# Kernel tuning notes

Measured on AMD Instinct MI355X. Metric: run time of the kernel, lower is better.

## Reference

```python
import jax, jax.numpy as jnp
import numpy as np

B, N, H = 8, 2048, 256


def setup_inputs() -> dict:
    key = jax.random.key(0)
    ks = jax.random.split(key, 8)
    s = 1.0 / np.sqrt(H)
    return {
        "node": jax.random.normal(ks[0], (B, N, H), dtype=jnp.float32),
        "graph": jax.random.uniform(ks[1], (B, N, N), dtype=jnp.float32),
        "W1": jax.random.normal(ks[2], (H, H), dtype=jnp.float32) * s,
        "b1": jnp.zeros((H,), dtype=jnp.float32),
        "W2": jax.random.normal(ks[3], (H, H), dtype=jnp.float32) * s,
        "b2": jnp.zeros((H,), dtype=jnp.float32),
        "Wout": jax.random.normal(ks[4], (H, 2 * H), dtype=jnp.float32) * (1.0 / np.sqrt(2 * H)),
        "bout": jnp.zeros((H,), dtype=jnp.float32),
    }


def reference(node, graph, W1, b1, W2, b2, Wout, bout):
    # Symmetric normalization D^{-1/2} A D^{-1/2}, batched and vectorized
    # (equivalent to the per-sample diag-mm loop in the original).
    d = jnp.sum(graph, axis=2)                # [B, N] row sums (torch sum(1) on [N,N])
    dinv = d ** -0.5                          # [B, N]
    g = graph * dinv[:, :, None] * dinv[:, None, :]  # [B, N, N]

    # node_info = relu(fc1(g @ node)); fc2(g @ node_info)
    h = jax.nn.relu(jnp.einsum("bnm,bmh->bnh", g, node) @ W1.T + b1)
    h = jax.nn.relu(jnp.einsum("bnm,bmh->bnh", g, h) @ W2.T + b2)

    agg = jnp.concatenate([node, h], axis=2)  # [B, N, 2H]
    return jax.nn.relu(agg @ Wout.T + bout)   # [B, N, H]
```

## Files before the change

kernel.cpp:

```cpp
#include <hip/hip_runtime.h>
#include <stdint.h>

typedef __attribute__((ext_vector_type(4))) float f32x4;
typedef __attribute__((ext_vector_type(8))) short bf16x8;

static __device__ __forceinline__ unsigned short f2bf(float x) {
  unsigned int u = __builtin_bit_cast(unsigned int, x);
  u = (u + 0x7fffu + ((u >> 16) & 1u)) >> 16;
  return (unsigned short)u;
}

#define GLD16(g, l)                                                            \
  __builtin_amdgcn_global_load_lds(                                            \
      (__attribute__((address_space(1))) const void*)(g),                      \
      (__attribute__((address_space(3))) void*)(l), 16, 0, 0)

__global__ __launch_bounds__(256) void rowscale_cvt_k(
    const float* __restrict__ g, float* __restrict__ dinv,
    unsigned short* __restrict__ gb) {
  int row = blockIdx.x * 4 + (threadIdx.x >> 6);
  int lane = threadIdx.x & 63;
  const float* p = g + (long)row * 2048;
  float4 v[8];
  float s = 0.f;
#pragma unroll
  for (int i = 0; i < 8; ++i) {
    v[i] = *(const float4*)(p + (lane + i * 64) * 4);
    s += v[i].x + v[i].y + v[i].z + v[i].w;
  }
#pragma unroll
  for (int off = 32; off; off >>= 1) s += __shfl_xor(s, off, 64);
  float di = rsqrtf(s);
  if (lane == 0) dinv[row] = di;
  unsigned short* q = gb + (long)row * 2048;
#pragma unroll
  for (int i = 0; i < 8; ++i) {
    ushort4 u;
    u.x = f2bf(v[i].x * di); u.y = f2bf(v[i].y * di);
    u.z = f2bf(v[i].z * di); u.w = f2bf(v[i].w * di);
    *(ushort4*)(q + (lane + i * 64) * 4) = u;
  }
}

__global__ __launch_bounds__(256) void cvt_w_k(const float* __restrict__ W1,
                                               const float* __restrict__ W2,
                                               const float* __restrict__ Wout,
                                               unsigned short* __restrict__ wb) {
  int idx = blockIdx.x * 256 + threadIdx.x;
  float v;
  if (idx < 65536) v = W1[idx];
  else if (idx < 131072) v = W2[idx - 65536];
  else v = Wout[idx - 131072];
  wb[idx] = f2bf(v);
}

__global__ __launch_bounds__(256) void prep_node_k(
    const float* __restrict__ node, const float* __restrict__ dinv,
    unsigned short* __restrict__ nodeT, unsigned short* __restrict__ agg) {
  __shared__ unsigned short t[64 * 68];
  int tid = threadIdx.x;
  int m0 = blockIdx.x * 64, h0 = blockIdx.y * 64;
  long b = blockIdx.z;
#pragma unroll
  for (int i = 0; i < 4; ++i) {
    int idx = tid + 256 * i;
    int r = idx >> 4, c4 = idx & 15;
    long m = m0 + r;
    float4 v = *(const float4*)(node + (b * 2048 + m) * 256 + h0 + c4 * 4);
    float di = dinv[b * 2048 + m];
    ushort4 u;
    u.x = f2bf(v.x); u.y = f2bf(v.y); u.z = f2bf(v.z); u.w = f2bf(v.w);
    *(ushort4*)(agg + (b * 2048 + m) * 512 + h0 + c4 * 4) = u;
    t[(c4 * 4 + 0) * 68 + r] = f2bf(v.x * di);
    t[(c4 * 4 + 1) * 68 + r] = f2bf(v.y * di);
    t[(c4 * 4 + 2) * 68 + r] = f2bf(v.z * di);
    t[(c4 * 4 + 3) * 68 + r] = f2bf(v.w * di);
  }
  __syncthreads();
#pragma unroll
  for (int i = 0; i < 4; ++i) {
    int idx = tid + 256 * i;
    int hr = idx >> 4, c4 = idx & 15;
    ushort4 o = *(const ushort4*)(&t[hr * 68 + c4 * 4]);
    *(ushort4*)(nodeT + (b * 256 + h0 + hr) * 2048 + m0 + c4 * 4) = o;
  }
}

template <bool BIAS, bool RELU, bool SCALE, bool TRANS, bool OUTF32>
__global__ __launch_bounds__(256, 2) void gemm_t(
    const unsigned short* __restrict__ A, const unsigned short* __restrict__ Bt,
    const float* __restrict__ bias, const float* __restrict__ scale,
    void* __restrict__ Cp, int K, int lda, int ldbt, long bBatch, int ldc) {
  __shared__ char lds[65536];
  char* ldsA = lds;
  char* ldsB = lds + 32768;

  int tid = threadIdx.x;
  int lane = tid & 63;
  int w = tid >> 6;
  int wm = w >> 1, wn = w & 1;

  int bid = blockIdx.x;
  int gt = ((bid & 7) << 5) + (bid >> 3);
  int mt = gt >> 1;
  int col0 = (gt & 1) * 128;
  long row0 = (long)mt * 128;
  int batch = mt >> 4;
  const unsigned short* Bb = Bt + (long)batch * bBatch;

  int nt = K >> 6;
  f32x4 acc[4][4] = {};

  auto stageA = [&](int kt, int buf) {
#pragma unroll
    for (int i = 0; i < 4; ++i) {
      int slot = i * 256 + tid;
      int r = slot >> 3, j = slot & 7;
      int jg = j ^ (r & 7);
      GLD16(A + (row0 + r) * (long)lda + kt * 64 + jg * 8,
            ldsA + buf * 16384 + (i * 4 + w) * 1024);
    }
  };
  auto stageB = [&](int kt, int buf) {
#pragma unroll
    for (int i = 0; i < 4; ++i) {
      int slot = i * 256 + tid;
      int c = slot >> 3, j = slot & 7;
      int jg = j ^ (c & 7);
      GLD16(Bb + (long)(col0 + c) * ldbt + kt * 64 + jg * 8,
            ldsB + buf * 16384 + (i * 4 + w) * 1024);
    }
  };
  auto compute = [&](int buf) {
    char* bA = ldsA + buf * 16384;
    char* bB = ldsB + buf * 16384;
    bf16x8 a[4][2], bb[4][2];
#pragma unroll
    for (int m = 0; m < 4; ++m)
#pragma unroll
      for (int kk = 0; kk < 2; ++kk) {
        int row = wm * 64 + m * 16 + (lane & 15);
        int off = (row * 128 + kk * 64 + (lane >> 4) * 16) ^ ((row & 7) << 4);
        a[m][kk] = *(const bf16x8*)(bA + off);
      }
#pragma unroll
    for (int n = 0; n < 4; ++n)
#pragma unroll
      for (int kk = 0; kk < 2; ++kk) {
        int col = wn * 64 + n * 16 + (lane & 15);
        int off = (col * 128 + kk * 64 + (lane >> 4) * 16) ^ ((col & 7) << 4);
        bb[n][kk] = *(const bf16x8*)(bB + off);
      }
#pragma unroll
    for (int m = 0; m < 4; ++m)
#pragma unroll
      for (int n = 0; n < 4; ++n) {
        acc[m][n] = __builtin_amdgcn_mfma_f32_16x16x32_bf16(a[m][0], bb[n][0],
                                                            acc[m][n], 0, 0, 0);
        acc[m][n] = __builtin_amdgcn_mfma_f32_16x16x32_bf16(a[m][1], bb[n][1],
                                                            acc[m][n], 0, 0, 0);
      }
  };

  stageA(0, 0);
  stageB(0, 0);
  __syncthreads();

  int cur = 0;
  for (int t = 0; t < nt; ++t) {
    int nxt = cur ^ 1;
    if (t + 1 < nt) {
      stageA(t + 1, nxt);
      stageB(t + 1, nxt);
    }
    compute(cur);
    __syncthreads();
    cur = nxt;
  }

  if (TRANS) {
    unsigned short* tb = (unsigned short*)lds;
#pragma unroll
    for (int m = 0; m < 4; ++m)
#pragma unroll
      for (int n = 0; n < 4; ++n) {
        int lc = wn * 64 + n * 16 + (lane & 15);
        float bv = BIAS ? bias[col0 + lc] : 0.f;
#pragma unroll
        for (int r = 0; r < 4; ++r) {
          int rl = wm * 64 + m * 16 + (lane >> 4) * 4 + r;
          float v = acc[m][n][r];
          if (BIAS) v += bv;
          if (RELU) v = fmaxf(v, 0.f);
          if (SCALE) v *= scale[row0 + rl];
          tb[lc * 136 + rl] = f2bf(v);
        }
      }
    __syncthreads();
    unsigned short* C = (unsigned short*)Cp;
    int rin = (int)(row0 & 2047);
#pragma unroll
    for (int i = 0; i < 8; ++i) {
      int id = i * 256 + tid;
      int lc = id >> 4, seg = id & 15;
      bf16x8 u = *(const bf16x8*)(tb + lc * 136 + seg * 8);
      *(bf16x8*)(C + ((long)batch * 256 + col0 + lc) * 2048 + rin + seg * 8) = u;
    }
  } else {
#pragma unroll
    for (int m = 0; m < 4; ++m)
#pragma unroll
      for (int n = 0; n < 4; ++n) {
        int col = col0 + wn * 64 + n * 16 + (lane & 15);
        float bv = BIAS ? bias[col] : 0.f;
#pragma unroll
        for (int r = 0; r < 4; ++r) {
          long row = row0 + wm * 64 + m * 16 + (lane >> 4) * 4 + r;
          float v = acc[m][n][r];
          if (BIAS) v += bv;
          if (RELU) v = fmaxf(v, 0.f);
          if (SCALE) v *= scale[row];
          if (OUTF32) ((float*)Cp)[row * ldc + col] = v;
          else ((unsigned short*)Cp)[row * ldc + col] = f2bf(v);
        }
      }
  }
}

extern "C" void kernel_launch(void* const* d_in, const int* in_sizes, int n_in,
                              void* d_out, int out_size, void* d_ws,
                              size_t ws_size, hipStream_t stream) {
  const float* node = (const float*)d_in[0];
  const float* graph = (const float*)d_in[1];
  const float* W1 = (const float*)d_in[2];
  const float* b1 = (const float*)d_in[3];
  const float* W2 = (const float*)d_in[4];
  const float* b2 = (const float*)d_in[5];
  const float* Wout = (const float*)d_in[6];
  const float* bout = (const float*)d_in[7];
  float* out = (float*)d_out;

  char* p = (char*)d_ws;
  float* dinv = (float*)p;                    p += 16384 * 4;
  unsigned short* wb = (unsigned short*)p;    p += 262144 * 2;
  unsigned short* gb = (unsigned short*)p;    p += 8L * 2048 * 2048 * 2;
  unsigned short* nodeT = (unsigned short*)p; p += 8L * 256 * 2048 * 2;
  unsigned short* bufT = (unsigned short*)p;  p += 8L * 2048 * 256 * 2;
  unsigned short* agg = (unsigned short*)p;   p += 8L * 2048 * 512 * 2;

  rowscale_cvt_k<<<4096, 256, 0, stream>>>(graph, dinv, gb);
  cvt_w_k<<<1024, 256, 0, stream>>>(W1, W2, Wout, wb);
  prep_node_k<<<dim3(32, 4, 8), 256, 0, stream>>>(node, dinv, nodeT, agg);

  gemm_t<false, false, false, false, false><<<256, 256, 0, stream>>>(
      gb, nodeT, nullptr, nullptr, bufT, 2048, 2048, 2048, 256L * 2048, 256);
  gemm_t<true, true, true, true, false><<<256, 256, 0, stream>>>(
      bufT, wb, b1, dinv, nodeT, 256, 256, 256, 0, 2048);
  gemm_t<false, false, false, false, false><<<256, 256, 0, stream>>>(
      gb, nodeT, nullptr, nullptr, bufT, 2048, 2048, 2048, 256L * 2048, 256);
  gemm_t<true, true, false, false, false><<<256, 256, 0, stream>>>(
      bufT, wb + 65536, b2, nullptr, agg + 256, 256, 256, 256, 0, 512);
  gemm_t<true, true, false, false, true><<<256, 256, 0, stream>>>(
      agg, wb + 131072, bout, nullptr, out, 512, 512, 512, 0, 256);
}
```

Before: 310.0 us.

## Fuse adjacency GEMM with following fc layer into one full-width kernel

Each graph-propagation GEMM (g @ X) is now fused with the following H×H linear layer in a single kernel, `mega_k`. It uses 64×256 row tiles with 512 threads, keeps the propagated tile in LDS as bf16 and applies bias, ReLU and the dinv scaling before writing. This removes the intermediate bufT global round trip and two kernel launches. The weight-conversion kernel is folded into the row-scale kernel as extra blocks. The final output GEMM becomes a specialised non-templated kernel. In exchange, each block runs the small second GEMM serially after the main loop without overlap, and occupancy drops to one 512-thread block per CU with a larger LDS footprint.

```diff
diff --git a/kernel.cpp b/kernel.cpp
--- a/kernel.cpp
+++ b/kernel.cpp
@@ -17,7 +17,22 @@
 
 __global__ __launch_bounds__(256) void rowscale_cvt_k(
     const float* __restrict__ g, float* __restrict__ dinv,
-    unsigned short* __restrict__ gb) {
+    unsigned short* __restrict__ gb, const float* __restrict__ W1,
+    const float* __restrict__ W2, const float* __restrict__ Wout,
+    unsigned short* __restrict__ wb) {
+  if (blockIdx.x >= 4096) {
+    int base = (blockIdx.x - 4096) * 2048;
+#pragma unroll
+    for (int i = 0; i < 8; ++i) {
+      int idx = base + i * 256 + threadIdx.x;
+      float v;
+      if (idx < 65536) v = W1[idx];
+      else if (idx < 131072) v = W2[idx - 65536];
+      else v = Wout[idx - 131072];
+      wb[idx] = f2bf(v);
+    }
+    return;
+  }
   int row = blockIdx.x * 4 + (threadIdx.x >> 6);
   int lane = threadIdx.x & 63;
   const float* p = g + (long)row * 2048;
@@ -40,18 +55,6 @@
     u.z = f2bf(v[i].z * di); u.w = f2bf(v[i].w * di);
     *(ushort4*)(q + (lane + i * 64) * 4) = u;
   }
-}
-
-__global__ __launch_bounds__(256) void cvt_w_k(const float* __restrict__ W1,
-                                               const float* __restrict__ W2,
-                                               const float* __restrict__ Wout,
-                                               unsigned short* __restrict__ wb) {
-  int idx = blockIdx.x * 256 + threadIdx.x;
-  float v;
-  if (idx < 65536) v = W1[idx];
-  else if (idx < 131072) v = W2[idx - 65536];
-  else v = Wout[idx - 131072];
-  wb[idx] = f2bf(v);
 }
 
 __global__ __launch_bounds__(256) void prep_node_k(
@@ -86,15 +89,195 @@
   }
 }
 
-template <bool BIAS, bool RELU, bool SCALE, bool TRANS, bool OUTF32>
-__global__ __launch_bounds__(256, 2) void gemm_t(
+template <bool TRANS_OUT>
+__global__ __launch_bounds__(512, 1) void mega_k(
     const unsigned short* __restrict__ A, const unsigned short* __restrict__ Bt,
-    const float* __restrict__ bias, const float* __restrict__ scale,
-    void* __restrict__ Cp, int K, int lda, int ldbt, long bBatch, int ldc) {
+    const unsigned short* __restrict__ W, const float* __restrict__ bias,
+    const float* __restrict__ dinv, unsigned short* __restrict__ Cout,
+    long bBatch) {
+  __shared__ char lds[81920];
+  char* ldsA = lds;
+  char* ldsB = lds + 16384;
+  char* ldsX = lds;
+  char* ldsW = lds + 32768;
+
+  int tid = threadIdx.x;
+  int lane = tid & 63;
+  int w = tid >> 6;
+  int wm = w >> 2, wn = w & 3;
+
+  int bid = blockIdx.x;
+  int batch = bid & 7;
+  int mt = bid >> 3;
+  long row0 = ((long)batch * 32 + mt) * 64;
+  const unsigned short* Bb = Bt + (long)batch * bBatch;
+
+  f32x4 acc[2][4] = {};
+
+  auto stageA = [&](int kt, int buf) {
+    int r = tid >> 3, j = tid & 7;
+    int jg = j ^ (r & 7);
+    GLD16(A + (row0 + r) * 2048 + kt * 64 + jg * 8,
+          ldsA + buf * 8192 + w * 1024);
+  };
+  auto stageB = [&](int kt, int buf) {
+#pragma unroll
+    for (int i = 0; i < 4; ++i) {
+      int slot = i * 512 + tid;
+      int c = slot >> 3, j = slot & 7;
+      int jg = j ^ (c & 7);
+      GLD16(Bb + (long)c * 2048 + kt * 64 + jg * 8,
+            ldsB + buf * 32768 + (i * 8 + w) * 1024);
+    }
+  };
+  auto compute1 = [&](int buf) {
+    char* bA = ldsA + buf * 8192;
+    char* bB = ldsB + buf * 32768;
+    bf16x8 a[2][2], bb[4][2];
+#pragma unroll
+    for (int m = 0; m < 2; ++m)
+#pragma unroll
+      for (int kk = 0; kk < 2; ++kk) {
+        int row = wm * 32 + m * 16 + (lane & 15);
+        int off = (row * 128 + kk * 64 + (lane >> 4) * 16) ^ ((row & 7) << 4);
+        a[m][kk] = *(const bf16x8*)(bA + off);
+      }
+#pragma unroll
+    for (int n = 0; n < 4; ++n)
+#pragma unroll
+      for (int kk = 0; kk < 2; ++kk) {
+        int col = wn * 64 + n * 16 + (lane & 15);
+        int off = (col * 128 + kk * 64 + (lane >> 4) * 16) ^ ((col & 7) << 4);
+        bb[n][kk] = *(const bf16x8*)(bB + off);
+      }
+#pragma unroll
+    for (int m = 0; m < 2; ++m)
+#pragma unroll
+      for (int n = 0; n < 4; ++n) {
+        acc[m][n] = __builtin_amdgcn_mfma_f32_16x16x32_bf16(a[m][0], bb[n][0],
+                                                            acc[m][n], 0, 0, 0);
+        acc[m][n] = __builtin_amdgcn_mfma_f32_16x16x32_bf16(a[m][1], bb[n][1],
+                                                            acc[m][n], 0, 0, 0);
+      }
+  };
+
+  stageA(0, 0);
+  stageB(0, 0);
+  __syncthreads();
+  int cur = 0;
+  for (int t = 0; t < 32; ++t) {
+    int nxt = cur ^ 1;
+    if (t + 1 < 32) {
+      stageA(t + 1, nxt);
+      stageB(t + 1, nxt);
+    }
+    compute1(cur);
+    __syncthreads();
+    cur = nxt;
+  }
+  __syncthreads();
+
+#pragma unroll
+  for (int m = 0; m < 2; ++m)
+#pragma unroll
+    for (int n = 0; n < 4; ++n) {
+      int col = wn * 64 + n * 16 + (lane & 15);
+#pragma unroll
+      for (int r = 0; r < 4; ++r) {
+        int row = wm * 32 + m * 16 + (lane >> 4) * 4 + r;
+        int off = (row * 512 + col * 2) ^ ((row & 7) << 4);
+        *(unsigned short*)(ldsX + off) = f2bf(acc[m][n][r]);
+      }
+    }
+
+  f32x4 acc2[2][4] = {};
+  for (int kt = 0; kt < 4; ++kt) {
+    __syncthreads();
+#pragma unroll
+    for (int i = 0; i < 4; ++i) {
+      int slot = i * 512 + tid;
+      int c = slot >> 3, j = slot & 7;
+      int jg = j ^ (c & 7);
+      GLD16(W + (long)c * 256 + kt * 64 + jg * 8, ldsW + (i * 8 + w) * 1024);
+    }
+    __syncthreads();
+    bf16x8 a[2][2], bb[4][2];
+#pragma unroll
+    for (int m = 0; m < 2; ++m)
+#pragma unroll
+      for (int kk = 0; kk < 2; ++kk) {
+        int row = wm * 32 + m * 16 + (lane & 15);
+        int off = (row * 512 + kt * 128 + kk * 64 + (lane >> 4) * 16) ^
+                  ((row & 7) << 4);
+        a[m][kk] = *(const bf16x8*)(ldsX + off);
+      }
+#pragma unroll
+    for (int n = 0; n < 4; ++n)
+#pragma unroll
+      for (int kk = 0; kk < 2; ++kk) {
+        int col = wn * 64 + n * 16 + (lane & 15);
+        int off = (col * 128 + kk * 64 + (lane >> 4) * 16) ^ ((col & 7) << 4);
+        bb[n][kk] = *(const bf16x8*)(ldsW + off);
+      }
+#pragma unroll
+    for (int m = 0; m < 2; ++m)
+#pragma unroll
+      for (int n = 0; n < 4; ++n) {
+        acc2[m][n] = __builtin_amdgcn_mfma_f32_16x16x32_bf16(a[m][0], bb[n][0],
+                                                             acc2[m][n], 0, 0, 0);
+        acc2[m][n] = __builtin_amdgcn_mfma_f32_16x16x32_bf16(a[m][1], bb[n][1],
+                                                             acc2[m][n], 0, 0, 0);
+      }
+  }
+
+  if (TRANS_OUT) {
+    __syncthreads();
+    unsigned short* tb = (unsigned short*)lds;
+#pragma unroll
+    for (int m = 0; m < 2; ++m)
+#pragma unroll
+      for (int n = 0; n < 4; ++n) {
+        int col = wn * 64 + n * 16 + (lane & 15);
+        float bv = bias[col];
+#pragma unroll
+        for (int r = 0; r < 4; ++r) {
+          int rl = wm * 32 + m * 16 + (lane >> 4) * 4 + r;
+          float v = fmaxf(acc2[m][n][r] + bv, 0.f) * dinv[row0 + rl];
+          tb[col * 72 + rl] = f2bf(v);
+        }
+      }
+    __syncthreads();
+    int rin = (int)(row0 & 2047);
+#pragma unroll
+    for (int i = 0; i < 4; ++i) {
+      int id = i * 512 + tid;
+      int col = id >> 3, seg = id & 7;
+      bf16x8 u = *(const bf16x8*)(tb + col * 72 + seg * 8);
+      *(bf16x8*)(Cout + ((long)batch * 256 + col) * 2048 + rin + seg * 8) = u;
+    }
+  } else {
+#pragma unroll
+    for (int m = 0; m < 2; ++m)
+#pragma unroll
+      for (int n = 0; n < 4; ++n) {
+        int col = wn * 64 + n * 16 + (lane & 15);
+        float bv = bias[col];
+#pragma unroll
+        for (int r = 0; r < 4; ++r) {
+          long row = row0 + wm * 32 + m * 16 + (lane >> 4) * 4 + r;
+          float v = fmaxf(acc2[m][n][r] + bv, 0.f);
+          Cout[row * 512 + col] = f2bf(v);
+        }
+      }
+  }
+}
+
+__global__ __launch_bounds__(256, 2) void gemm_f3(
+    const unsigned short* __restrict__ A, const unsigned short* __restrict__ Bt,
+    const float* __restrict__ bias, float* __restrict__ C) {
   __shared__ char lds[65536];
   char* ldsA = lds;
   char* ldsB = lds + 32768;
-
   int tid = threadIdx.x;
   int lane = tid & 63;
   int w = tid >> 6;
@@ -105,19 +288,15 @@
   int mt = gt >> 1;
   int col0 = (gt & 1) * 128;
   long row0 = (long)mt * 128;
-  int batch = mt >> 4;
-  const unsigned short* Bb = Bt + (long)batch * bBatch;
-
-  int nt = K >> 6;
+
   f32x4 acc[4][4] = {};
-
   auto stageA = [&](int kt, int buf) {
 #pragma unroll
     for (int i = 0; i < 4; ++i) {
       int slot = i * 256 + tid;
       int r = slot >> 3, j = slot & 7;
       int jg = j ^ (r & 7);
-      GLD16(A + (row0 + r) * (long)lda + kt * 64 + jg * 8,
+      GLD16(A + (row0 + r) * 512 + kt * 64 + jg * 8,
             ldsA + buf * 16384 + (i * 4 + w) * 1024);
     }
   };
@@ -127,7 +306,7 @@
       int slot = i * 256 + tid;
       int c = slot >> 3, j = slot & 7;
       int jg = j ^ (c & 7);
-      GLD16(Bb + (long)(col0 + c) * ldbt + kt * 64 + jg * 8,
+      GLD16(Bt + (long)(col0 + c) * 512 + kt * 64 + jg * 8,
             ldsB + buf * 16384 + (i * 4 + w) * 1024);
     }
   };
@@ -165,11 +344,10 @@
   stageA(0, 0);
   stageB(0, 0);
   __syncthreads();
-
   int cur = 0;
-  for (int t = 0; t < nt; ++t) {
+  for (int t = 0; t < 8; ++t) {
     int nxt = cur ^ 1;
-    if (t + 1 < nt) {
+    if (t + 1 < 8) {
       stageA(t + 1, nxt);
       stageB(t + 1, nxt);
     }
@@ -177,54 +355,18 @@
     __syncthreads();
     cur = nxt;
   }
-
-  if (TRANS) {
-    unsigned short* tb = (unsigned short*)lds;
-#pragma unroll
-    for (int m = 0; m < 4; ++m)
-#pragma unroll
-      for (int n = 0; n < 4; ++n) {
-        int lc = wn * 64 + n * 16 + (lane & 15);
-        float bv = BIAS ? bias[col0 + lc] : 0.f;
-#pragma unroll
-        for (int r = 0; r < 4; ++r) {
-          int rl = wm * 64 + m * 16 + (lane >> 4) * 4 + r;
-          float v = acc[m][n][r];
-          if (BIAS) v += bv;
-          if (RELU) v = fmaxf(v, 0.f);
-          if (SCALE) v *= scale[row0 + rl];
-          tb[lc * 136 + rl] = f2bf(v);
-        }
-      }
-    __syncthreads();
-    unsigned short* C = (unsigned short*)Cp;
-    int rin = (int)(row0 & 2047);
-#pragma unroll
-    for (int i = 0; i < 8; ++i) {
-      int id = i * 256 + tid;
-      int lc = id >> 4, seg = id & 15;
-      bf16x8 u = *(const bf16x8*)(tb + lc * 136 + seg * 8);
-      *(bf16x8*)(C + ((long)batch * 256 + col0 + lc) * 2048 + rin + seg * 8) = u;
-    }
-  } else {
-#pragma unroll
-    for (int m = 0; m < 4; ++m)
-#pragma unroll
-      for (int n = 0; n < 4; ++n) {
-        int col = col0 + wn * 64 + n * 16 + (lane & 15);
-        float bv = BIAS ? bias[col] : 0.f;
-#pragma unroll
-        for (int r = 0; r < 4; ++r) {
-          long row = row0 + wm * 64 + m * 16 + (lane >> 4) * 4 + r;
-          float v = acc[m][n][r];
-          if (BIAS) v += bv;
-          if (RELU) v = fmaxf(v, 0.f);
-          if (SCALE) v *= scale[row];
-          if (OUTF32) ((float*)Cp)[row * ldc + col] = v;
-          else ((unsigned short*)Cp)[row * ldc + col] = f2bf(v);
-        }
-      }
-  }
+#pragma unroll
+  for (int m = 0; m < 4; ++m)
+#pragma unroll
+    for (int n = 0; n < 4; ++n) {
+      int col = col0 + wn * 64 + n * 16 + (lane & 15);
+      float bv = bias[col & 255];
+#pragma unroll
+      for (int r = 0; r < 4; ++r) {
+        long row = row0 + wm * 64 + m * 16 + (lane >> 4) * 4 + r;
+        C[row * 256 + (col & 255)] = fmaxf(acc[m][n][r] + bv, 0.f);
+      }
+    }
 }
 
 extern "C" void kernel_launch(void* const* d_in, const int* in_sizes, int n_in,
@@ -245,21 +387,14 @@
   unsigned short* wb = (unsigned short*)p;    p += 262144 * 2;
   unsigned short* gb = (unsigned short*)p;    p += 8L * 2048 * 2048 * 2;
   unsigned short* nodeT = (unsigned short*)p; p += 8L * 256 * 2048 * 2;
-  unsigned short* bufT = (unsigned short*)p;  p += 8L * 2048 * 256 * 2;
+  unsigned short* xT = (unsigned short*)p;    p += 8L * 256 * 2048 * 2;
   unsigned short* agg = (unsigned short*)p;   p += 8L * 2048 * 512 * 2;
 
-  rowscale_cvt_k<<<4096, 256, 0, stream>>>(graph, dinv, gb);
-  cvt_w_k<<<1024, 256, 0, stream>>>(W1, W2, Wout, wb);
+  rowscale_cvt_k<<<4224, 256, 0, stream>>>(graph, dinv, gb, W1, W2, Wout, wb);
   prep_node_k<<<dim3(32, 4, 8), 256, 0, stream>>>(node, dinv, nodeT, agg);
-
-  gemm_t<false, false, false, false, false><<<256, 256, 0, stream>>>(
-      gb, nodeT, nullptr, nullptr, bufT, 2048, 2048, 2048, 256L * 2048, 256);
-  gemm_t<true, true, true, true, false><<<256, 256, 0, stream>>>(
-      bufT, wb, b1, dinv, nodeT, 256, 256, 256, 0, 2048);
-  gemm_t<false, false, false, false, false><<<256, 256, 0, stream>>>(
-      gb, nodeT, nullptr, nullptr, bufT, 2048, 2048, 2048, 256L * 2048, 256);
-  gemm_t<true, true, false, false, false><<<256, 256, 0, stream>>>(
-      bufT, wb + 65536, b2, nullptr, agg + 256, 256, 256, 256, 0, 512);
-  gemm_t<true, true, false, false, true><<<256, 256, 0, stream>>>(
-      agg, wb + 131072, bout, nullptr, out, 512, 512, 512, 0, 256);
-}
+  mega_k<true><<<256, 512, 0, stream>>>(gb, nodeT, wb, b1, dinv, xT,
+                                        256L * 2048);
+  mega_k<false><<<256, 512, 0, stream>>>(gb, xT, wb + 65536, b2, dinv,
+                                         agg + 256, 256L * 2048);
+  gemm_f3<<<256, 256, 0, stream>>>(agg, wb + 131072, bout, out);
+}
```

After: 310.4 us. No clear change (+0.1%).
